# Performance work log

Hardware: AMD Instinct MI355X
Metric: run time of the kernel (lower is better)

Reference implementation:

```python
import jax, jax.numpy as jnp
import numpy as np
from jax import lax

B, L, DDYN, DSTAT, H = 512, 64, 16, 8, 512
N_BANK, C_CAND, K_TOP, N_PROTO = 50000, 1024, 16, 8
T_TARG, Q_QUANT = 2, 3
TEMP = 0.2


def _l2norm(x, eps=1e-12):
    # matches torch.nn.functional.normalize: x / max(||x||, eps)
    n = jnp.sqrt(jnp.sum(x * x, axis=-1, keepdims=True))
    return x / jnp.maximum(n, eps)


def setup_inputs() -> dict:
    key = jax.random.key(0)
    ks = jax.random.split(key, 24)
    s = 0.02
    inp = {
        'sequence_values': jax.random.normal(ks[0], (B, L, DDYN), jnp.float32),
        'sequence_masks': jnp.ones((B, L), jnp.float32),
        'static_values': jax.random.normal(ks[1], (B, DSTAT), jnp.float32),
        'bank_keys': jax.random.normal(ks[2], (N_BANK, H), jnp.float32),
        'bank_values': jax.random.normal(ks[3], (N_BANK, H), jnp.float32),
        'candidate_indices': jax.random.randint(ks[4], (B, C_CAND), 0, N_BANK, jnp.int64),
        # encoder params (SequenceEncoder stand-in: masked-mean + linear + relu)
        'W_seq': jax.random.normal(ks[5], (DDYN, H), jnp.float32) * s,
        'W_stat': jax.random.normal(ks[6], (DSTAT, H), jnp.float32) * s,
        'b_enc': jnp.zeros((H,), jnp.float32),
        # retrieval / prototype / fusion params
        'W_q': jax.random.normal(ks[7], (H, H), jnp.float32) * s,
        'b_q': jnp.zeros((H,), jnp.float32),
        'prototype_tokens': jax.random.normal(ks[8], (N_PROTO, H), jnp.float32) * 0.02,
        'W_tr': jax.random.normal(ks[9], (2 * H, H), jnp.float32) * s,
        'b_tr': jnp.zeros((H,), jnp.float32),
        'W_gate': jax.random.normal(ks[10], (3 * H, H), jnp.float32) * s,
        'b_gate': jnp.zeros((H,), jnp.float32),
        'W_out': jax.random.normal(ks[11], (H, H), jnp.float32) * s,
        'b_out': jnp.zeros((H,), jnp.float32),
        # per-target heads stacked: [T, H, Q] and [T, H]
        'W_quant': jax.random.normal(ks[12], (T_TARG, H, Q_QUANT), jnp.float32) * s,
        'b_quant': jnp.zeros((T_TARG, Q_QUANT), jnp.float32),
        'W_ev': jax.random.normal(ks[13], (T_TARG, H), jnp.float32) * s,
        'b_ev': jnp.zeros((T_TARG,), jnp.float32),
    }
    return inp


def reference(sequence_values, sequence_masks, static_values, bank_keys, bank_values,
              candidate_indices, W_seq, W_stat, b_enc, W_q, b_q, prototype_tokens,
              W_tr, b_tr, W_gate, b_gate, W_out, b_out, W_quant, b_quant, W_ev, b_ev):
    # --- encoder (masked mean pool + linear + relu stand-in for SequenceEncoder) ---
    m = sequence_masks[..., None]                                   # [B,L,1]
    pooled = (sequence_values * m).sum(1) / jnp.maximum(m.sum(1), 1e-6)
    local_hidden = jax.nn.relu(pooled @ W_seq + static_values @ W_stat + b_enc)  # [B,H]

    # --- normalized query ---
    query = _l2norm(local_hidden @ W_q + b_q)                       # [B,H]

    # --- donor retrieval: gather + dot + topk + softmax + weighted sum ---
    cand_keys = bank_keys[candidate_indices]                        # [B,C,H]
    sim = jnp.einsum('bch,bh->bc', cand_keys, query)                # [B,C]
    top_scores, top_pos = lax.top_k(sim, K_TOP)                     # [B,K]
    weights = jax.nn.softmax(top_scores / max(TEMP, 1e-6), axis=-1)
    sel_idx = jnp.take_along_axis(candidate_indices, top_pos, axis=1)  # [B,K]
    donor_hidden = jnp.einsum('bk,bkh->bh', weights, bank_values[sel_idx])

    # --- prototype attention ---
    protos_n = _l2norm(prototype_tokens)                            # [P,H]
    pw = jax.nn.softmax(query @ protos_n.T, axis=-1)                # [B,P]
    proto_hidden = pw @ prototype_tokens                            # [B,H]

    # --- transfer / gate / fuse (dropout is identity at eval) ---
    transfer = jax.nn.relu(jnp.concatenate([donor_hidden, proto_hidden], -1) @ W_tr + b_tr)
    gate = jax.nn.sigmoid(
        jnp.concatenate([local_hidden, donor_hidden, proto_hidden], -1) @ W_gate + b_gate)
    fused = gate * local_hidden + (1.0 - gate) * transfer
    fused = jax.nn.relu(fused @ W_out + b_out)                      # [B,H]

    # --- heads: sorted quantiles [B,T,Q] and event logits [B,T] ---
    quant = jnp.sort(jnp.einsum('bh,thq->btq', fused, W_quant) + b_quant, axis=-1)
    logit = jnp.einsum('bh,th->bt', fused, W_ev) + b_ev
    return jnp.concatenate([quant.reshape(quant.shape[0], -1), logit], axis=-1)  # [B, T*Q+T]
```

## Files before the change

### kernel.cpp

```cpp
#include <hip/hip_runtime.h>
#include <hip/hip_bf16.h>

typedef __hip_bfloat16 bf16;

__device__ __forceinline__ float lo16(unsigned u){ return __uint_as_float(u << 16); }
__device__ __forceinline__ float hi16(unsigned u){ return __uint_as_float(u & 0xffff0000u); }

#define Bn 512
#define Hn 512
#define Cn 1024
#define Kn 16
#define NBANK 50000

__device__ __forceinline__ int clamp_id(int id){
    return (id < 0) ? 0 : ((id >= NBANK) ? (NBANK - 1) : id);
}

#define QRAW_OFF 0
#define G_OFF    262144
#define SIM_OFF  1048576
#define F1_OFF   1572864
#define F2_OFF   1835008
#define WS_FLOATS 2097152

__global__ __launch_bounds__(256) void k_enc(
    const float* __restrict__ seq, const float* __restrict__ mask, const float* __restrict__ stat,
    const float* __restrict__ W_seq, const float* __restrict__ W_stat, const float* __restrict__ b_enc,
    float* __restrict__ ws)
{
    const int b = blockIdx.x, t = threadIdx.x;
    const int h0 = 2*t, h1 = 2*t + 1;
    __shared__ float s_pool[16], s_stat[8];
    if (t < 16) {
        float acc = 0.f, ms = 0.f;
        for (int l = 0; l < 64; l++) {
            float m = mask[b*64 + l];
            ms  += m;
            acc += seq[(b*64 + l)*16 + t] * m;
        }
        s_pool[t] = acc / fmaxf(ms, 1e-6f);
    } else if (t < 24) {
        s_stat[t - 16] = stat[b*8 + (t - 16)];
    }
    __syncthreads();
    float a0 = b_enc[h0], a1 = b_enc[h1];
    #pragma unroll
    for (int j = 0; j < 16; j++) {
        float2 wv = *(const float2*)(W_seq + j*Hn + h0);
        a0 += s_pool[j]*wv.x; a1 += s_pool[j]*wv.y;
    }
    #pragma unroll
    for (int j = 0; j < 8; j++) {
        float2 wv = *(const float2*)(W_stat + j*Hn + h0);
        a0 += s_stat[j]*wv.x; a1 += s_stat[j]*wv.y;
    }
    float* g = ws + G_OFF + (size_t)b*1536;
    g[h0] = fmaxf(a0, 0.f); g[h1] = fmaxf(a1, 0.f);
}

__global__ __launch_bounds__(256) void k_qgemm(
    const float* __restrict__ W_q, const float* __restrict__ b_q, float* __restrict__ ws)
{
    const int ct = blockIdx.x, rt = blockIdx.y, t = threadIdx.x;
    const int col = ct*64 + (t & 63), rg = t >> 6;
    __shared__ float lt[16][520];
    {
        int r = t >> 4, koff = (t & 15)*32;
        const float* src = ws + G_OFF + (size_t)(rt*16 + r)*1536 + koff;
        #pragma unroll
        for (int i = 0; i < 8; i++)
            *(float4*)&lt[r][koff + i*4] = *(const float4*)(src + i*4);
    }
    __syncthreads();
    float acc[4]; float bq = b_q[col];
    #pragma unroll
    for (int i = 0; i < 4; i++) acc[i] = bq;
    #pragma unroll 4
    for (int k = 0; k < 512; k += 2) {
        float w0 = W_q[(size_t)k*Hn + col], w1 = W_q[(size_t)(k+1)*Hn + col];
        #pragma unroll
        for (int i = 0; i < 4; i++) {
            float2 gv = *(const float2*)&lt[rg*4 + i][k];
            acc[i] += gv.x*w0 + gv.y*w1;
        }
    }
    #pragma unroll
    for (int i = 0; i < 4; i++)
        ws[QRAW_OFF + (size_t)(rt*16 + rg*4 + i)*Hn + col] = acc[i];
}

__global__ __launch_bounds__(256) void k_sim(
    const float* __restrict__ bank_keys, const int* __restrict__ cand32,
    float* __restrict__ ws)
{
    const int chunk = blockIdx.x, b = blockIdx.y, t = threadIdx.x;
    const int w = t >> 6, lane = t & 63;
    const int c64 = ((cand32[1] | cand32[3] | cand32[5] | cand32[7]) == 0) ? 1 : 0;

    const float* qr = ws + QRAW_OFF + (size_t)b*Hn + lane*8;
    float4 qa = *(const float4*)qr, qb = *(const float4*)(qr + 4);
    float ss = qa.x*qa.x + qa.y*qa.y + qa.z*qa.z + qa.w*qa.w
             + qb.x*qb.x + qb.y*qb.y + qb.z*qb.z + qb.w*qb.w;
    #pragma unroll
    for (int o = 32; o; o >>= 1) ss += __shfl_xor(ss, o);
    float inv = 1.f / fmaxf(sqrtf(ss), 1e-12f);
    float qv[8] = {qa.x*inv, qa.y*inv, qa.z*inv, qa.w*inv,
                   qb.x*inv, qb.y*inv, qb.z*inv, qb.w*inv};

    const int cbase = b*Cn + chunk*128 + w*32;
    float* simrow = ws + SIM_OFF + (size_t)b*Cn + chunk*128 + w*32;
    for (int g8 = 0; g8 < 32; g8 += 8) {
        float4 ka[8], kb2[8];
        #pragma unroll
        for (int u = 0; u < 8; u++) {
            int id = clamp_id(cand32[(size_t)(cbase + g8 + u) << c64]);
            const float* kp = bank_keys + (size_t)id*Hn + lane*8;
            ka[u]  = *(const float4*)kp;
            kb2[u] = *(const float4*)(kp + 4);
        }
        #pragma unroll
        for (int u = 0; u < 8; u++) {
            float s = ka[u].x*qv[0] + ka[u].y*qv[1] + ka[u].z*qv[2] + ka[u].w*qv[3]
                    + kb2[u].x*qv[4] + kb2[u].y*qv[5] + kb2[u].z*qv[6] + kb2[u].w*qv[7];
            #pragma unroll
            for (int o = 32; o; o >>= 1) s += __shfl_xor(s, o);
            if (lane == 0) simrow[g8 + u] = s;
        }
    }
}

__global__ __launch_bounds__(256) void k_select(
    const float* __restrict__ bank_values, const int* __restrict__ cand32,
    const float* __restrict__ proto, float* __restrict__ ws)
{
    const int b = blockIdx.x, t = threadIdx.x;
    const int w = t >> 6, lane = t & 63;
    const int h0 = 2*t, h1 = 2*t + 1;
    const int c64 = ((cand32[1] | cand32[3] | cand32[5] | cand32[7]) == 0) ? 1 : 0;

    __shared__ __align__(16) float s_sim[Cn];
    __shared__ float s_bv[4]; __shared__ int s_bi[4];
    __shared__ float s_topv[Kn]; __shared__ int s_sel[Kn];
    __shared__ float s_w[Kn];
    __shared__ float s_score[8], s_pw[8];

    *(float4*)&s_sim[t*4] = *(const float4*)(ws + SIM_OFF + (size_t)b*Cn + t*4);

    const float* qr = ws + QRAW_OFF + (size_t)b*Hn + lane*8;
    float4 qa = *(const float4*)qr, qb = *(const float4*)(qr + 4);
    float ss = qa.x*qa.x + qa.y*qa.y + qa.z*qa.z + qa.w*qa.w
             + qb.x*qb.x + qb.y*qb.y + qb.z*qb.z + qb.w*qb.w;
    #pragma unroll
    for (int o = 32; o; o >>= 1) ss += __shfl_xor(ss, o);
    float qinv = 1.f / fmaxf(sqrtf(ss), 1e-12f);
    float qv[8] = {qa.x*qinv, qa.y*qinv, qa.z*qinv, qa.w*qinv,
                   qb.x*qinv, qb.y*qinv, qb.z*qinv, qb.w*qinv};
    __syncthreads();

    for (int k = 0; k < Kn; k++) {
        float best = -1e30f; int bi = 0x7fffffff;
        for (int i = t; i < Cn; i += 256) {
            float v = s_sim[i];
            if (v > best || (v == best && i < bi)) { best = v; bi = i; }
        }
        #pragma unroll
        for (int o = 32; o; o >>= 1) {
            float ov = __shfl_xor(best, o); int oi = __shfl_xor(bi, o);
            if (ov > best || (ov == best && oi < bi)) { best = ov; bi = oi; }
        }
        if (lane == 0) { s_bv[w] = best; s_bi[w] = bi; }
        __syncthreads();
        if (t == 0) {
            float bv = s_bv[0]; int bbi = s_bi[0];
            for (int x = 1; x < 4; x++)
                if (s_bv[x] > bv || (s_bv[x] == bv && s_bi[x] < bbi)) { bv = s_bv[x]; bbi = s_bi[x]; }
            if (bbi < 0 || bbi >= Cn) bbi = 0;
            s_topv[k] = bv; s_sel[k] = bbi; s_sim[bbi] = -1e30f;
        }
        __syncthreads();
    }

    if (t == 0) {
        float m = s_topv[0];
        float e[Kn], ssum = 0.f;
        for (int k = 0; k < Kn; k++) { e[k] = __expf((s_topv[k] - m) * 5.0f); ssum += e[k]; }
        float inv = 1.f / ssum;
        for (int k = 0; k < Kn; k++) s_w[k] = e[k] * inv;
    }
    for (int p = w; p < 8; p += 4) {
        const float* pp = proto + (size_t)p*Hn + lane*8;
        float4 pa = *(const float4*)pp, pb = *(const float4*)(pp + 4);
        float f[8] = {pa.x, pa.y, pa.z, pa.w, pb.x, pb.y, pb.z, pb.w};
        float dq = 0.f, sq = 0.f;
        #pragma unroll
        for (int i = 0; i < 8; i++) { dq += f[i]*qv[i]; sq += f[i]*f[i]; }
        #pragma unroll
        for (int o = 32; o; o >>= 1) { dq += __shfl_xor(dq, o); sq += __shfl_xor(sq, o); }
        if (lane == 0) s_score[p] = dq / fmaxf(sqrtf(sq), 1e-12f);
    }
    __syncthreads();
    if (t == 0) {
        float m = s_score[0];
        for (int p = 1; p < 8; p++) m = fmaxf(m, s_score[p]);
        float e[8], ssum = 0.f;
        for (int p = 0; p < 8; p++) { e[p] = __expf(s_score[p] - m); ssum += e[p]; }
        float inv = 1.f / ssum;
        for (int p = 0; p < 8; p++) s_pw[p] = e[p] * inv;
    }
    __syncthreads();

    float* g = ws + G_OFF + (size_t)b*1536;
    {
        float a0 = 0.f, a1 = 0.f;
        #pragma unroll
        for (int k = 0; k < Kn; k++) {
            int id = clamp_id(cand32[(size_t)(b*Cn + s_sel[k]) << c64]);
            float2 v = *(const float2*)(bank_values + (size_t)id*Hn + h0);
            a0 += s_w[k]*v.x; a1 += s_w[k]*v.y;
        }
        g[512 + h0] = a0; g[512 + h1] = a1;
    }
    {
        float a0 = 0.f, a1 = 0.f;
        #pragma unroll
        for (int p = 0; p < 8; p++) {
            float2 v = *(const float2*)(proto + (size_t)p*Hn + h0);
            a0 += s_pw[p]*v.x; a1 += s_pw[p]*v.y;
        }
        g[1024 + h0] = a0; g[1024 + h1] = a1;
    }
}

__global__ __launch_bounds__(256) void k_f1(
    const float* __restrict__ W_tr, const float* __restrict__ b_tr,
    const float* __restrict__ W_gate, const float* __restrict__ b_gate,
    float* __restrict__ ws)
{
    const int ct = blockIdx.x, rt = blockIdx.y, t = threadIdx.x;
    const int col = ct*64 + (t & 63), rg = t >> 6;
    __shared__ float lt[16][520];
    float accg[4], acct[4];
    float bg = b_gate[col], bt = b_tr[col];
    #pragma unroll
    for (int i = 0; i < 4; i++) { accg[i] = bg; acct[i] = bt; }

    for (int kt = 0; kt < 3; kt++) {
        {
            int r = t >> 4, koff = (t & 15)*32;
            const float* src = ws + G_OFF + (size_t)(rt*16 + r)*1536 + kt*512 + koff;
            #pragma unroll
            for (int i = 0; i < 8; i++)
                *(float4*)&lt[r][koff + i*4] = *(const float4*)(src + i*4);
        }
        __syncthreads();
        if (kt == 0) {
            #pragma unroll 4
            for (int k = 0; k < 512; k += 2) {
                float w0 = W_gate[(size_t)k*Hn + col], w1 = W_gate[(size_t)(k+1)*Hn + col];
                #pragma unroll
                for (int i = 0; i < 4; i++) {
                    float2 gv = *(const float2*)&lt[rg*4 + i][k];
                    accg[i] += gv.x*w0 + gv.y*w1;
                }
            }
        } else {
            const int kg = kt*512, ktr = (kt-1)*512;
            #pragma unroll 4
            for (int k = 0; k < 512; k += 2) {
                float wg0 = W_gate[(size_t)(kg+k)*Hn + col], wg1 = W_gate[(size_t)(kg+k+1)*Hn + col];
                float wt0 = W_tr[(size_t)(ktr+k)*Hn + col],  wt1 = W_tr[(size_t)(ktr+k+1)*Hn + col];
                #pragma unroll
                for (int i = 0; i < 4; i++) {
                    float2 gv = *(const float2*)&lt[rg*4 + i][k];
                    accg[i] += gv.x*wg0 + gv.y*wg1;
                    acct[i] += gv.x*wt0 + gv.y*wt1;
                }
            }
        }
        __syncthreads();
    }
    #pragma unroll
    for (int i = 0; i < 4; i++) {
        int row = rt*16 + rg*4 + i;
        float lcl = ws[G_OFF + (size_t)row*1536 + col];
        float gate = 1.f/(1.f + __expf(-accg[i]));
        float tr = fmaxf(acct[i], 0.f);
        ws[F1_OFF + (size_t)row*Hn + col] = gate*lcl + (1.f - gate)*tr;
    }
}

__global__ __launch_bounds__(256) void k_f2(
    const float* __restrict__ W_out, const float* __restrict__ b_out, float* __restrict__ ws)
{
    const int ct = blockIdx.x, rt = blockIdx.y, t = threadIdx.x;
    const int col = ct*64 + (t & 63), rg = t >> 6;
    __shared__ float lt[16][520];
    {
        int r = t >> 4, koff = (t & 15)*32;
        const float* src = ws + F1_OFF + (size_t)(rt*16 + r)*Hn + koff;
        #pragma unroll
        for (int i = 0; i < 8; i++)
            *(float4*)&lt[r][koff + i*4] = *(const float4*)(src + i*4);
    }
    __syncthreads();
    float acc[4]; float bo = b_out[col];
    #pragma unroll
    for (int i = 0; i < 4; i++) acc[i] = bo;
    #pragma unroll 4
    for (int k = 0; k < 512; k += 2) {
        float w0 = W_out[(size_t)k*Hn + col], w1 = W_out[(size_t)(k+1)*Hn + col];
        #pragma unroll
        for (int i = 0; i < 4; i++) {
            float2 gv = *(const float2*)&lt[rg*4 + i][k];
            acc[i] += gv.x*w0 + gv.y*w1;
        }
    }
    #pragma unroll
    for (int i = 0; i < 4; i++)
        ws[F2_OFF + (size_t)(rt*16 + rg*4 + i)*Hn + col] = fmaxf(acc[i], 0.f);
}

__global__ __launch_bounds__(64) void k_heads(
    const float* __restrict__ W_quant, const float* __restrict__ b_quant,
    const float* __restrict__ W_ev, const float* __restrict__ b_ev,
    const float* __restrict__ ws_ro, float* __restrict__ out)
{
    const int b = blockIdx.x, lane = threadIdx.x;
    const float* fr = ws_ro + F2_OFF + (size_t)b*Hn + lane*8;
    float4 fa = *(const float4*)fr, fb = *(const float4*)(fr + 4);
    float fv[8] = {fa.x, fa.y, fa.z, fa.w, fb.x, fb.y, fb.z, fb.w};
    float acc[8];
    #pragma unroll
    for (int o = 0; o < 8; o++) acc[o] = 0.f;
    #pragma unroll
    for (int i = 0; i < 8; i++) {
        int h = lane*8 + i;
        float fh = fv[i];
        acc[0] += fh*W_quant[(0*Hn + h)*3 + 0];
        acc[1] += fh*W_quant[(0*Hn + h)*3 + 1];
        acc[2] += fh*W_quant[(0*Hn + h)*3 + 2];
        acc[3] += fh*W_quant[(1*Hn + h)*3 + 0];
        acc[4] += fh*W_quant[(1*Hn + h)*3 + 1];
        acc[5] += fh*W_quant[(1*Hn + h)*3 + 2];
        acc[6] += fh*W_ev[0*Hn + h];
        acc[7] += fh*W_ev[1*Hn + h];
    }
    #pragma unroll
    for (int o = 0; o < 8; o++) {
        #pragma unroll
        for (int s = 32; s; s >>= 1) acc[o] += __shfl_xor(acc[o], s);
    }
    if (lane == 0) {
        float q[6];
        for (int o = 0; o < 6; o++) q[o] = acc[o] + b_quant[o];
        #pragma unroll
        for (int tt = 0; tt < 2; tt++) {
            float a = q[tt*3], bb = q[tt*3+1], c = q[tt*3+2];
            float mn = fminf(a, fminf(bb, c)), mx = fmaxf(a, fmaxf(bb, c));
            float md = a + bb + c - mn - mx;
            q[tt*3] = mn; q[tt*3+1] = md; q[tt*3+2] = mx;
        }
        for (int o = 0; o < 6; o++) out[b*8 + o] = q[o];
        out[b*8 + 6] = acc[6] + b_ev[0];
        out[b*8 + 7] = acc[7] + b_ev[1];
    }
}

__device__ __forceinline__ float lds_f(const void* p, int i, int f32){
    return f32 ? ((const float*)p)[i] : __bfloat162float(((const bf16*)p)[i]);
}
__device__ __forceinline__ float2 ldpair(const void* p, int elt, int f32){
    if (f32) return ((const float2*)p)[elt >> 1];
    unsigned u = ((const unsigned*)p)[elt >> 1];
    return make_float2(lo16(u), hi16(u));
}
__device__ __forceinline__ void ld8(const void* p, int elt, int f32, float* v){
    if (f32){
        const float4* q = (const float4*)((const float*)p + elt);
        float4 a = q[0], b = q[1];
        v[0]=a.x; v[1]=a.y; v[2]=a.z; v[3]=a.w; v[4]=b.x; v[5]=b.y; v[6]=b.z; v[7]=b.w;
    } else {
        uint4 u = *(const uint4*)((const bf16*)p + elt);
        v[0]=lo16(u.x); v[1]=hi16(u.x); v[2]=lo16(u.y); v[3]=hi16(u.y);
        v[4]=lo16(u.z); v[5]=hi16(u.z); v[6]=lo16(u.w); v[7]=hi16(u.w);
    }
}
__device__ __forceinline__ void st_out(void* o, int i, int f32, float v){
    if (f32) ((float*)o)[i] = v; else ((bf16*)o)[i] = __float2bfloat16(v);
}

__global__ __launch_bounds__(256) void k_fused(
    const void* __restrict__ seq, const void* __restrict__ mask, const void* __restrict__ stat,
    const void* __restrict__ bank_keys, const void* __restrict__ bank_values,
    const int* __restrict__ cand32,
    const void* __restrict__ W_seq, const void* __restrict__ W_stat, const void* __restrict__ b_enc,
    const void* __restrict__ W_q, const void* __restrict__ b_q,
    const void* __restrict__ proto,
    const void* __restrict__ W_tr, const void* __restrict__ b_tr,
    const void* __restrict__ W_gate, const void* __restrict__ b_gate,
    const void* __restrict__ W_out, const void* __restrict__ b_out,
    const void* __restrict__ W_quant, const void* __restrict__ b_quant,
    const void* __restrict__ W_ev, const void* __restrict__ b_ev,
    void* __restrict__ out)
{
    const int b = blockIdx.x, t = threadIdx.x;
    const int w = t >> 6, lane = t & 63;
    const int h0 = 2*t, h1 = 2*t + 1;
    const int f32 = (((const unsigned short*)mask)[0] == 0) ? 1 : 0;
    const int c64 = ((cand32[1] | cand32[3] | cand32[5] | cand32[7]) == 0) ? 1 : 0;

    __shared__ __align__(16) float s_pool[16];
    __shared__ __align__(16) float s_stat[8];
    __shared__ __align__(16) float g[1536];
    __shared__ __align__(16) float s_q[Hn];
    __shared__ __align__(16) float s_sim[Cn];
    __shared__ __align__(16) float f1[Hn];
    __shared__ __align__(16) float f2[Hn];
    __shared__ float s_part[4], s_ss;
    __shared__ float s_bv[4]; __shared__ int s_bi[4];
    __shared__ float s_topv[Kn]; __shared__ int s_sel[Kn];
    __shared__ float s_w[Kn];
    __shared__ float s_score[8], s_pw[8];
    __shared__ float s_head[8][4];

    if (t < 16) {
        float acc = 0.f, ms = 0.f;
        for (int l = 0; l < 64; l++) {
            float m = lds_f(mask, b*64 + l, f32);
            ms  += m;
            acc += lds_f(seq, (b*64 + l)*16 + t, f32) * m;
        }
        s_pool[t] = acc / fmaxf(ms, 1e-6f);
    } else if (t < 24) {
        s_stat[t - 16] = lds_f(stat, b*8 + (t - 16), f32);
    }
    __syncthreads();
    {
        float a0 = lds_f(b_enc, h0, f32), a1 = lds_f(b_enc, h1, f32);
        #pragma unroll
        for (int j = 0; j < 16; j++) {
            float2 wv = ldpair(W_seq, j*Hn + h0, f32);
            a0 += s_pool[j]*wv.x; a1 += s_pool[j]*wv.y;
        }
        #pragma unroll
        for (int j = 0; j < 8; j++) {
            float2 wv = ldpair(W_stat, j*Hn + h0, f32);
            a0 += s_stat[j]*wv.x; a1 += s_stat[j]*wv.y;
        }
        a0 = fmaxf(a0, 0.f); a1 = fmaxf(a1, 0.f);
        g[h0] = a0; g[h1] = a1;
    }
    __syncthreads();
    {
        float q0 = lds_f(b_q, h0, f32), q1 = lds_f(b_q, h1, f32);
        #pragma unroll 4
        for (int j = 0; j < Hn; j++) {
            float lj = g[j];
            float2 wv = ldpair(W_q, j*Hn + h0, f32);
            q0 += lj*wv.x; q1 += lj*wv.y;
        }
        float ss = q0*q0 + q1*q1;
        #pragma unroll
        for (int o = 32; o; o >>= 1) ss += __shfl_xor(ss, o);
        if (lane == 0) s_part[w] = ss;
        __syncthreads();
        if (t == 0) s_ss = s_part[0] + s_part[1] + s_part[2] + s_part[3];
        __syncthreads();
        float inv = 1.f / fmaxf(sqrtf(s_ss), 1e-12f);
        s_q[h0] = q0*inv; s_q[h1] = q1*inv;
    }
    __syncthreads();
    float qv[8];
    #pragma unroll
    for (int i = 0; i < 8; i++) qv[i] = s_q[lane*8 + i];

    for (int c0 = w*256; c0 < w*256 + 256; c0 += 4) {
        float kf[4][8];
        #pragma unroll
        for (int u = 0; u < 4; u++) {
            int id = clamp_id(cand32[(size_t)(b*Cn + c0 + u) << c64]);
            ld8(bank_keys, id*Hn + lane*8, f32, kf[u]);
        }
        #pragma unroll
        for (int u = 0; u < 4; u++) {
            float s = 0.f;
            #pragma unroll
            for (int i = 0; i < 8; i++) s += kf[u][i]*qv[i];
            #pragma unroll
            for (int o = 32; o; o >>= 1) s += __shfl_xor(s, o);
            if (lane == 0) s_sim[c0 + u] = s;
        }
    }
    __syncthreads();
    for (int k = 0; k < Kn; k++) {
        float best = -1e30f; int bi = 0x7fffffff;
        for (int i = t; i < Cn; i += 256) {
            float v = s_sim[i];
            if (v > best || (v == best && i < bi)) { best = v; bi = i; }
        }
        #pragma unroll
        for (int o = 32; o; o >>= 1) {
            float ov = __shfl_xor(best, o); int oi = __shfl_xor(bi, o);
            if (ov > best || (ov == best && oi < bi)) { best = ov; bi = oi; }
        }
        if (lane == 0) { s_bv[w] = best; s_bi[w] = bi; }
        __syncthreads();
        if (t == 0) {
            float bv = s_bv[0]; int bbi = s_bi[0];
            for (int x = 1; x < 4; x++)
                if (s_bv[x] > bv || (s_bv[x] == bv && s_bi[x] < bbi)) { bv = s_bv[x]; bbi = s_bi[x]; }
            if (bbi < 0 || bbi >= Cn) bbi = 0;
            s_topv[k] = bv; s_sel[k] = bbi; s_sim[bbi] = -1e30f;
        }
        __syncthreads();
    }
    if (t == 0) {
        float m = s_topv[0];
        float e[Kn], ssum = 0.f;
        for (int k = 0; k < Kn; k++) { e[k] = __expf((s_topv[k] - m) * 5.0f); ssum += e[k]; }
        float inv = 1.f / ssum;
        for (int k = 0; k < Kn; k++) s_w[k] = e[k] * inv;
    }
    __syncthreads();
    {
        float a0 = 0.f, a1 = 0.f;
        #pragma unroll
        for (int k = 0; k < Kn; k++) {
            int id = clamp_id(cand32[(size_t)(b*Cn + s_sel[k]) << c64]);
            float2 v = ldpair(bank_values, id*Hn + h0, f32);
            a0 += s_w[k]*v.x; a1 += s_w[k]*v.y;
        }
        g[512 + h0] = a0; g[512 + h1] = a1;
    }
    for (int p = w; p < 8; p += 4) {
        float f[8];
        ld8(proto, p*Hn + lane*8, f32, f);
        float dq = 0.f, sq = 0.f;
        #pragma unroll
        for (int i = 0; i < 8; i++) { dq += f[i]*qv[i]; sq += f[i]*f[i]; }
        #pragma unroll
        for (int o = 32; o; o >>= 1) { dq += __shfl_xor(dq, o); sq += __shfl_xor(sq, o); }
        if (lane == 0) s_score[p] = dq / fmaxf(sqrtf(sq), 1e-12f);
    }
    __syncthreads();
    if (t == 0) {
        float m = s_score[0];
        for (int p = 1; p < 8; p++) m = fmaxf(m, s_score[p]);
        float e[8], ssum = 0.f;
        for (int p = 0; p < 8; p++) { e[p] = __expf(s_score[p] - m); ssum += e[p]; }
        float inv = 1.f / ssum;
        for (int p = 0; p < 8; p++) s_pw[p] = e[p] * inv;
    }
    __syncthreads();
    {
        float a0 = 0.f, a1 = 0.f;
        #pragma unroll
        for (int p = 0; p < 8; p++) {
            float2 v = ldpair(proto, p*Hn + h0, f32);
            a0 += s_pw[p]*v.x; a1 += s_pw[p]*v.y;
        }
        g[1024 + h0] = a0; g[1024 + h1] = a1;
    }
    __syncthreads();
    float tr0 = lds_f(b_tr, h0, f32), tr1 = lds_f(b_tr, h1, f32);
    #pragma unroll 4
    for (int j = 0; j < 1024; j++) {
        float gj = g[512 + j];
        float2 wv = ldpair(W_tr, j*Hn + h0, f32);
        tr0 += gj*wv.x; tr1 += gj*wv.y;
    }
    tr0 = fmaxf(tr0, 0.f); tr1 = fmaxf(tr1, 0.f);
    float gt0 = lds_f(b_gate, h0, f32), gt1 = lds_f(b_gate, h1, f32);
    #pragma unroll 4
    for (int j = 0; j < 1536; j++) {
        float gj = g[j];
        float2 wv = ldpair(W_gate, j*Hn + h0, f32);
        gt0 += gj*wv.x; gt1 += gj*wv.y;
    }
    gt0 = 1.f/(1.f + __expf(-gt0)); gt1 = 1.f/(1.f + __expf(-gt1));
    f1[h0] = gt0*g[h0] + (1.f - gt0)*tr0;
    f1[h1] = gt1*g[h1] + (1.f - gt1)*tr1;
    __syncthreads();
    {
        float o0 = lds_f(b_out, h0, f32), o1 = lds_f(b_out, h1, f32);
        #pragma unroll 4
        for (int j = 0; j < Hn; j++) {
            float fj = f1[j];
            float2 wv = ldpair(W_out, j*Hn + h0, f32);
            o0 += fj*wv.x; o1 += fj*wv.y;
        }
        o0 = fmaxf(o0, 0.f); o1 = fmaxf(o1, 0.f);
        f2[h0] = o0; f2[h1] = o1;
    }
    __syncthreads();
    {
        float acc[8];
        #pragma unroll
        for (int o = 0; o < 8; o++) acc[o] = 0.f;
        for (int h = t; h < Hn; h += 256) {
            float fh = f2[h];
            acc[0] += fh*lds_f(W_quant, (0*Hn + h)*3 + 0, f32);
            acc[1] += fh*lds_f(W_quant, (0*Hn + h)*3 + 1, f32);
            acc[2] += fh*lds_f(W_quant, (0*Hn + h)*3 + 2, f32);
            acc[3] += fh*lds_f(W_quant, (1*Hn + h)*3 + 0, f32);
            acc[4] += fh*lds_f(W_quant, (1*Hn + h)*3 + 1, f32);
            acc[5] += fh*lds_f(W_quant, (1*Hn + h)*3 + 2, f32);
            acc[6] += fh*lds_f(W_ev, 0*Hn + h, f32);
            acc[7] += fh*lds_f(W_ev, 1*Hn + h, f32);
        }
        #pragma unroll
        for (int o = 0; o < 8; o++) {
            float v = acc[o];
            #pragma unroll
            for (int s = 32; s; s >>= 1) v += __shfl_xor(v, s);
            if (lane == 0) s_head[o][w] = v;
        }
        __syncthreads();
        if (t == 0) {
            float q[6];
            for (int o = 0; o < 6; o++)
                q[o] = s_head[o][0] + s_head[o][1] + s_head[o][2] + s_head[o][3] + lds_f(b_quant, o, f32);
            #pragma unroll
            for (int tt = 0; tt < 2; tt++) {
                float a = q[tt*3], bb = q[tt*3+1], c = q[tt*3+2];
                float mn = fminf(a, fminf(bb, c)), mx = fmaxf(a, fmaxf(bb, c));
                float md = a + bb + c - mn - mx;
                q[tt*3] = mn; q[tt*3+1] = md; q[tt*3+2] = mx;
            }
            for (int o = 0; o < 6; o++) st_out(out, b*8 + o, f32, q[o]);
            float l0 = s_head[6][0] + s_head[6][1] + s_head[6][2] + s_head[6][3] + lds_f(b_ev, 0, f32);
            float l1 = s_head[7][0] + s_head[7][1] + s_head[7][2] + s_head[7][3] + lds_f(b_ev, 1, f32);
            st_out(out, b*8 + 6, f32, l0);
            st_out(out, b*8 + 7, f32, l1);
        }
    }
}

extern "C" void kernel_launch(void* const* d_in, const int* in_sizes, int n_in,
                              void* d_out, int out_size, void* d_ws, size_t ws_size,
                              hipStream_t stream) {
    static const int expect[22] = {
        512*64*16, 512*64, 512*8, 50000*512, 50000*512, 512*1024,
        16*512, 8*512, 512, 512*512, 512, 8*512,
        1024*512, 512, 1536*512, 512, 512*512, 512,
        2*512*3, 2*3, 2*512, 2
    };
    if (n_in != 22 || out_size != 512*8) return;
    for (int i = 0; i < 22; i++) if (in_sizes[i] != expect[i]) return;

    if (ws_size < (size_t)WS_FLOATS * 4) {
        k_fused<<<Bn, 256, 0, stream>>>(
            d_in[0], d_in[1], d_in[2], d_in[3], d_in[4], (const int*)d_in[5],
            d_in[6], d_in[7], d_in[8], d_in[9], d_in[10], d_in[11],
            d_in[12], d_in[13], d_in[14], d_in[15], d_in[16], d_in[17],
            d_in[18], d_in[19], d_in[20], d_in[21], d_out);
        return;
    }

    float* ws = (float*)d_ws;
    k_enc<<<Bn, 256, 0, stream>>>((const float*)d_in[0], (const float*)d_in[1],
                                  (const float*)d_in[2], (const float*)d_in[6],
                                  (const float*)d_in[7], (const float*)d_in[8], ws);
    k_qgemm<<<dim3(8, 32), 256, 0, stream>>>((const float*)d_in[9], (const float*)d_in[10], ws);
    k_sim<<<dim3(8, Bn), 256, 0, stream>>>((const float*)d_in[3], (const int*)d_in[5], ws);
    k_select<<<Bn, 256, 0, stream>>>((const float*)d_in[4], (const int*)d_in[5],
                                     (const float*)d_in[11], ws);
    k_f1<<<dim3(8, 32), 256, 0, stream>>>((const float*)d_in[12], (const float*)d_in[13],
                                          (const float*)d_in[14], (const float*)d_in[15], ws);
    k_f2<<<dim3(8, 32), 256, 0, stream>>>((const float*)d_in[16], (const float*)d_in[17], ws);
    k_heads<<<Bn, 64, 0, stream>>>((const float*)d_in[18], (const float*)d_in[19],
                                   (const float*)d_in[20], (const float*)d_in[21],
                                   ws, (float*)d_out);
}
```

Before: 618.2 us.

## Split-K the dense GEMMs with atomic accumulation and register-tiled 4x4 outputs

Replaces the row-tiled GEMMs for the query projection, gate/transfer, and output layers with split-K kernels. Each kernel computes 4x4 register tiles from float4 weight loads and accumulates partial sums into zeroed buffers with atomicAdd. The gate/transfer epilogue moves into a separate elementwise kernel, and the output ReLU moves into the heads kernel. The goal is more blocks and better weight reuse for small GEMMs. The cost is extra memsets, an extra launch, atomic traffic, and a floating-point summation order that is no longer deterministic.

After: 546.2 us. 11.7% less time.

```diff
diff --git a/kernel.cpp b/kernel.cpp
--- a/kernel.cpp
+++ b/kernel.cpp
@@ -17,10 +17,12 @@
 }
 
 #define QRAW_OFF 0
+#define F1_OFF   0
 #define G_OFF    262144
 #define SIM_OFF  1048576
-#define F1_OFF   1572864
-#define F2_OFF   1835008
+#define F2_OFF   1048576
+#define GATE_OFF 1572864
+#define TR_OFF   1835008
 #define WS_FLOATS 2097152
 
 __global__ __launch_bounds__(256) void k_enc(
@@ -58,35 +60,47 @@
     g[h0] = fmaxf(a0, 0.f); g[h1] = fmaxf(a1, 0.f);
 }
 
-__global__ __launch_bounds__(256) void k_qgemm(
-    const float* __restrict__ W_q, const float* __restrict__ b_q, float* __restrict__ ws)
-{
-    const int ct = blockIdx.x, rt = blockIdx.y, t = threadIdx.x;
-    const int col = ct*64 + (t & 63), rg = t >> 6;
-    __shared__ float lt[16][520];
-    {
-        int r = t >> 4, koff = (t & 15)*32;
-        const float* src = ws + G_OFF + (size_t)(rt*16 + r)*1536 + koff;
+__global__ __launch_bounds__(256) void k_qgemm_sk(
+    const float* __restrict__ W, const float* __restrict__ bias,
+    const float* __restrict__ in, int in_stride, int in_off,
+    float* __restrict__ outp)
+{
+    const int ct = blockIdx.x, rt = blockIdx.y, kz = blockIdx.z, t = threadIdx.x;
+    __shared__ float lt[64][132];
+    {
+        int r = t >> 2, c0 = (t & 3)*32;
+        const float* src = in + (size_t)(rt*64 + r)*in_stride + in_off + kz*128 + c0;
         #pragma unroll
         for (int i = 0; i < 8; i++)
-            *(float4*)&lt[r][koff + i*4] = *(const float4*)(src + i*4);
-    }
-    __syncthreads();
-    float acc[4]; float bq = b_q[col];
-    #pragma unroll
-    for (int i = 0; i < 4; i++) acc[i] = bq;
+            *(float4*)&lt[r][c0 + i*4] = *(const float4*)(src + i*4);
+    }
+    __syncthreads();
+    const int col0 = ct*64 + (t & 15)*4, rbase = (t >> 4)*4;
+    float acc[4][4];
+    if (kz == 0) {
+        float4 bv = *(const float4*)(bias + col0);
+        #pragma unroll
+        for (int i = 0; i < 4; i++) { acc[i][0]=bv.x; acc[i][1]=bv.y; acc[i][2]=bv.z; acc[i][3]=bv.w; }
+    } else {
+        #pragma unroll
+        for (int i = 0; i < 4; i++) { acc[i][0]=0; acc[i][1]=0; acc[i][2]=0; acc[i][3]=0; }
+    }
+    const float* wp = W + (size_t)(kz*128)*Hn + col0;
     #pragma unroll 4
-    for (int k = 0; k < 512; k += 2) {
-        float w0 = W_q[(size_t)k*Hn + col], w1 = W_q[(size_t)(k+1)*Hn + col];
+    for (int k = 0; k < 128; k++) {
+        float4 wv = *(const float4*)(wp + (size_t)k*Hn);
         #pragma unroll
         for (int i = 0; i < 4; i++) {
-            float2 gv = *(const float2*)&lt[rg*4 + i][k];
-            acc[i] += gv.x*w0 + gv.y*w1;
-        }
-    }
-    #pragma unroll
-    for (int i = 0; i < 4; i++)
-        ws[QRAW_OFF + (size_t)(rt*16 + rg*4 + i)*Hn + col] = acc[i];
+            float a = lt[rbase + i][k];
+            acc[i][0] += a*wv.x; acc[i][1] += a*wv.y; acc[i][2] += a*wv.z; acc[i][3] += a*wv.w;
+        }
+    }
+    #pragma unroll
+    for (int i = 0; i < 4; i++) {
+        float* op = outp + (size_t)(rt*64 + rbase + i)*Hn + col0;
+        atomicAdd(op+0, acc[i][0]); atomicAdd(op+1, acc[i][1]);
+        atomicAdd(op+2, acc[i][2]); atomicAdd(op+3, acc[i][3]);
+    }
 }
 
 __global__ __launch_bounds__(256) void k_sim(
@@ -231,93 +245,70 @@
     }
 }
 
-__global__ __launch_bounds__(256) void k_f1(
+__global__ __launch_bounds__(256) void k_gatetr_sk(
     const float* __restrict__ W_tr, const float* __restrict__ b_tr,
     const float* __restrict__ W_gate, const float* __restrict__ b_gate,
     float* __restrict__ ws)
 {
-    const int ct = blockIdx.x, rt = blockIdx.y, t = threadIdx.x;
-    const int col = ct*64 + (t & 63), rg = t >> 6;
-    __shared__ float lt[16][520];
-    float accg[4], acct[4];
-    float bg = b_gate[col], bt = b_tr[col];
-    #pragma unroll
-    for (int i = 0; i < 4; i++) { accg[i] = bg; acct[i] = bt; }
-
-    for (int kt = 0; kt < 3; kt++) {
-        {
-            int r = t >> 4, koff = (t & 15)*32;
-            const float* src = ws + G_OFF + (size_t)(rt*16 + r)*1536 + kt*512 + koff;
-            #pragma unroll
-            for (int i = 0; i < 8; i++)
-                *(float4*)&lt[r][koff + i*4] = *(const float4*)(src + i*4);
-        }
-        __syncthreads();
-        if (kt == 0) {
-            #pragma unroll 4
-            for (int k = 0; k < 512; k += 2) {
-                float w0 = W_gate[(size_t)k*Hn + col], w1 = W_gate[(size_t)(k+1)*Hn + col];
-                #pragma unroll
-                for (int i = 0; i < 4; i++) {
-                    float2 gv = *(const float2*)&lt[rg*4 + i][k];
-                    accg[i] += gv.x*w0 + gv.y*w1;
-                }
-            }
-        } else {
-            const int kg = kt*512, ktr = (kt-1)*512;
-            #pragma unroll 4
-            for (int k = 0; k < 512; k += 2) {
-                float wg0 = W_gate[(size_t)(kg+k)*Hn + col], wg1 = W_gate[(size_t)(kg+k+1)*Hn + col];
-                float wt0 = W_tr[(size_t)(ktr+k)*Hn + col],  wt1 = W_tr[(size_t)(ktr+k+1)*Hn + col];
-                #pragma unroll
-                for (int i = 0; i < 4; i++) {
-                    float2 gv = *(const float2*)&lt[rg*4 + i][k];
-                    accg[i] += gv.x*wg0 + gv.y*wg1;
-                    acct[i] += gv.x*wt0 + gv.y*wt1;
-                }
-            }
-        }
-        __syncthreads();
+    const int ct = blockIdx.x, rt = blockIdx.y, z = blockIdx.z, t = threadIdx.x;
+    const int isGate = (z < 6);
+    const int slice = isGate ? z : (z - 6);
+    const float* W  = isGate ? W_gate : W_tr;
+    const int inoff = (isGate ? 0 : 512) + slice*256;
+    float* outp = ws + (isGate ? GATE_OFF : TR_OFF);
+
+    __shared__ float lt[32][260];
+    {
+        int r = t >> 3, c0 = (t & 7)*32;
+        const float* src = ws + G_OFF + (size_t)(rt*32 + r)*1536 + inoff + c0;
+        #pragma unroll
+        for (int i = 0; i < 8; i++)
+            *(float4*)&lt[r][c0 + i*4] = *(const float4*)(src + i*4);
+    }
+    __syncthreads();
+    const int col0 = ct*128 + (t & 31)*4, rbase = (t >> 5)*4;
+    float acc[4][4];
+    if (slice == 0) {
+        const float* bias = isGate ? b_gate : b_tr;
+        float4 bv = *(const float4*)(bias + col0);
+        #pragma unroll
+        for (int i = 0; i < 4; i++) { acc[i][0]=bv.x; acc[i][1]=bv.y; acc[i][2]=bv.z; acc[i][3]=bv.w; }
+    } else {
+        #pragma unroll
+        for (int i = 0; i < 4; i++) { acc[i][0]=0; acc[i][1]=0; acc[i][2]=0; acc[i][3]=0; }
+    }
+    const float* wp = W + (size_t)(slice*256)*Hn + col0;
+    #pragma unroll 4
+    for (int k = 0; k < 256; k++) {
+        float4 wv = *(const float4*)(wp + (size_t)k*Hn);
+        #pragma unroll
+        for (int i = 0; i < 4; i++) {
+            float a = lt[rbase + i][k];
+            acc[i][0] += a*wv.x; acc[i][1] += a*wv.y; acc[i][2] += a*wv.z; acc[i][3] += a*wv.w;
+        }
     }
     #pragma unroll
     for (int i = 0; i < 4; i++) {
-        int row = rt*16 + rg*4 + i;
-        float lcl = ws[G_OFF + (size_t)row*1536 + col];
-        float gate = 1.f/(1.f + __expf(-accg[i]));
-        float tr = fmaxf(acct[i], 0.f);
-        ws[F1_OFF + (size_t)row*Hn + col] = gate*lcl + (1.f - gate)*tr;
-    }
-}
-
-__global__ __launch_bounds__(256) void k_f2(
-    const float* __restrict__ W_out, const float* __restrict__ b_out, float* __restrict__ ws)
-{
-    const int ct = blockIdx.x, rt = blockIdx.y, t = threadIdx.x;
-    const int col = ct*64 + (t & 63), rg = t >> 6;
-    __shared__ float lt[16][520];
-    {
-        int r = t >> 4, koff = (t & 15)*32;
-        const float* src = ws + F1_OFF + (size_t)(rt*16 + r)*Hn + koff;
-        #pragma unroll
-        for (int i = 0; i < 8; i++)
-            *(float4*)&lt[r][koff + i*4] = *(const float4*)(src + i*4);
-    }
-    __syncthreads();
-    float acc[4]; float bo = b_out[col];
-    #pragma unroll
-    for (int i = 0; i < 4; i++) acc[i] = bo;
-    #pragma unroll 4
-    for (int k = 0; k < 512; k += 2) {
-        float w0 = W_out[(size_t)k*Hn + col], w1 = W_out[(size_t)(k+1)*Hn + col];
-        #pragma unroll
-        for (int i = 0; i < 4; i++) {
-            float2 gv = *(const float2*)&lt[rg*4 + i][k];
-            acc[i] += gv.x*w0 + gv.y*w1;
-        }
-    }
-    #pragma unroll
-    for (int i = 0; i < 4; i++)
-        ws[F2_OFF + (size_t)(rt*16 + rg*4 + i)*Hn + col] = fmaxf(acc[i], 0.f);
+        float* op = outp + (size_t)(rt*32 + rbase + i)*Hn + col0;
+        atomicAdd(op+0, acc[i][0]); atomicAdd(op+1, acc[i][1]);
+        atomicAdd(op+2, acc[i][2]); atomicAdd(op+3, acc[i][3]);
+    }
+}
+
+__global__ __launch_bounds__(256) void k_f1ew(float* __restrict__ ws)
+{
+    const int i4 = blockIdx.x*256 + threadIdx.x;
+    const int row = i4 >> 7, c = (i4 & 127)*4;
+    float4 lc = *(const float4*)(ws + G_OFF + (size_t)row*1536 + c);
+    float4 ga = *(const float4*)(ws + GATE_OFF + (size_t)row*Hn + c);
+    float4 tr = *(const float4*)(ws + TR_OFF + (size_t)row*Hn + c);
+    float4 r;
+    float s;
+    s = 1.f/(1.f + __expf(-ga.x)); r.x = s*lc.x + (1.f-s)*fmaxf(tr.x, 0.f);
+    s = 1.f/(1.f + __expf(-ga.y)); r.y = s*lc.y + (1.f-s)*fmaxf(tr.y, 0.f);
+    s = 1.f/(1.f + __expf(-ga.z)); r.z = s*lc.z + (1.f-s)*fmaxf(tr.z, 0.f);
+    s = 1.f/(1.f + __expf(-ga.w)); r.w = s*lc.w + (1.f-s)*fmaxf(tr.w, 0.f);
+    *(float4*)(ws + F1_OFF + (size_t)row*Hn + c) = r;
 }
 
 __global__ __launch_bounds__(64) void k_heads(
@@ -328,7 +319,8 @@
     const int b = blockIdx.x, lane = threadIdx.x;
     const float* fr = ws_ro + F2_OFF + (size_t)b*Hn + lane*8;
     float4 fa = *(const float4*)fr, fb = *(const float4*)(fr + 4);
-    float fv[8] = {fa.x, fa.y, fa.z, fa.w, fb.x, fb.y, fb.z, fb.w};
+    float fv[8] = {fmaxf(fa.x,0.f), fmaxf(fa.y,0.f), fmaxf(fa.z,0.f), fmaxf(fa.w,0.f),
+                   fmaxf(fb.x,0.f), fmaxf(fb.y,0.f), fmaxf(fb.z,0.f), fmaxf(fb.w,0.f)};
     float acc[8];
     #pragma unroll
     for (int o = 0; o < 8; o++) acc[o] = 0.f;
@@ -658,16 +650,24 @@
     }
 
     float* ws = (float*)d_ws;
+    hipMemsetAsync(ws + QRAW_OFF, 0, (size_t)512*512*4, stream);
+    hipMemsetAsync(ws + GATE_OFF, 0, (size_t)2*512*512*4, stream);
+
     k_enc<<<Bn, 256, 0, stream>>>((const float*)d_in[0], (const float*)d_in[1],
                                   (const float*)d_in[2], (const float*)d_in[6],
                                   (const float*)d_in[7], (const float*)d_in[8], ws);
-    k_qgemm<<<dim3(8, 32), 256, 0, stream>>>((const float*)d_in[9], (const float*)d_in[10], ws);
+    k_qgemm_sk<<<dim3(8, 8, 4), 256, 0, stream>>>(
+        (const float*)d_in[9], (const float*)d_in[10], ws + G_OFF, 1536, 0, ws + QRAW_OFF);
     k_sim<<<dim3(8, Bn), 256, 0, stream>>>((const float*)d_in[3], (const int*)d_in[5], ws);
     k_select<<<Bn, 256, 0, stream>>>((const float*)d_in[4], (const int*)d_in[5],
                                      (const float*)d_in[11], ws);
-    k_f1<<<dim3(8, 32), 256, 0, stream>>>((const float*)d_in[12], (const float*)d_in[13],
-                                          (const float*)d_in[14], (const float*)d_in[15], ws);
-    k_f2<<<dim3(8, 32), 256, 0, stream>>>((const float*)d_in[16], (const float*)d_in[17], ws);
+    hipMemsetAsync(ws + F2_OFF, 0, (size_t)512*512*4, stream);
+    k_gatetr_sk<<<dim3(4, 16, 10), 256, 0, stream>>>(
+        (const float*)d_in[12], (const float*)d_in[13],
+        (const float*)d_in[14], (const float*)d_in[15], ws);
+    k_f1ew<<<256, 256, 0, stream>>>(ws);
+    k_qgemm_sk<<<dim3(8, 8, 4), 256, 0, stream>>>(
+        (const float*)d_in[16], (const float*)d_in[17], ws + F1_OFF, 512, 0, ws + F2_OFF);
     k_heads<<<Bn, 64, 0, stream>>>((const float*)d_in[18], (const float*)d_in[19],
                                    (const float*)d_in[20], (const float*)d_in[21],
                                    ws, (float*)d_out);
```
